# Optimization experiments

Measured on AMD Instinct MI355X. Metric: run time of the kernel, lower is better.

## Reference

```python
import jax, jax.numpy as jnp
import numpy as np

COMMITMENT_COST = 0.25


def setup_inputs() -> dict:
    key = jax.random.key(0)
    k1, k2 = jax.random.split(key)
    x = jax.random.normal(k1, (4, 64, 32, 32, 32), dtype=jnp.float32)
    weight = jax.random.normal(k2, (512, 64), dtype=jnp.float32)
    return {"x": x, "weight": weight}


def reference(x, weight):
    b, c, h, w, d = x.shape  # c == embed_dim
    # [b, h, w, d, c] -> [N, c]
    flat = jnp.transpose(x, (0, 2, 3, 4, 1)).reshape(-1, c)
    # squared L2 distances to each codebook vector: [N, n_embed]
    distances = (
        jnp.sum(flat * flat, axis=1, keepdims=True)
        - 2.0 * (flat @ weight.T)
        + jnp.sum(weight * weight, axis=1)
    )
    embed_idx_flat = jnp.argmin(distances, axis=1)  # == argmax(-distances)
    embed_idx = embed_idx_flat.reshape(b, h, w, d)
    # gather codebook rows and move embed dim back to channel position
    quantized = jnp.transpose(weight[embed_idx], (0, 4, 1, 2, 3))  # [b, c, h, w, d]
    latent_loss = COMMITMENT_COST * jnp.mean(
        (jax.lax.stop_gradient(quantized) - x) ** 2
    )
    quantized_st = jax.lax.stop_gradient(quantized - x) + x
    return quantized_st, embed_idx, latent_loss
```

## Files before the change

### kernel.cpp

```cpp
#include <hip/hip_runtime.h>
#include <hip/hip_bf16.h>

#define HWD      32768
#define NC       64
#define NE       512
#define OUT_IDX  8388608
#define OUT_LOSS 8519680

#define WS_WSQ_F   16
#define WS_SLOT_F  528
#define WS_WP_B    4096
#define WS_NEEDED  200704

typedef __attribute__((ext_vector_type(8))) short bf16x8;
typedef __attribute__((ext_vector_type(4))) float f32x4;

__device__ inline unsigned short bf16_rne(float v) {
    unsigned u = __builtin_bit_cast(unsigned, v);
    return (unsigned short)((u + 0x7FFFu + ((u >> 16) & 1u)) >> 16);
}
__device__ inline float bf16_f(unsigned short s) {
    return __builtin_bit_cast(float, (unsigned)s << 16);
}
__device__ inline void split3(float v, unsigned short& h, unsigned short& m,
                              unsigned short& l) {
    h = bf16_rne(v);
    float r1 = v - bf16_f(h);
    m = bf16_rne(r1);
    float r2 = r1 - bf16_f(m);
    l = bf16_rne(r2);
}

__global__ __launch_bounds__(256) void vq_prep(
    const float* __restrict__ w, float* __restrict__ ws)
{
    const int gtid = blockIdx.x * 256 + threadIdx.x;
    if (gtid == 0) { ws[0] = 0.f; ((unsigned*)ws)[1] = 0u; }
    if (gtid < 256) ws[WS_SLOT_F + gtid] = 0.f;
    if (gtid < NE) {
        const float4* row = (const float4*)(w + (size_t)gtid * NC);
        float s0 = 0.f, s1 = 0.f, s2 = 0.f, s3 = 0.f;
#pragma unroll
        for (int k = 0; k < 16; ++k) {
            float4 v = row[k];
            s0 = fmaf(v.x, v.x, s0); s1 = fmaf(v.y, v.y, s1);
            s2 = fmaf(v.z, v.z, s2); s3 = fmaf(v.w, v.w, s3);
        }
        ws[WS_WSQ_F + gtid] = (s0 + s1) + (s2 + s3);
    }
    const int lane_s = gtid & 63;
    int t = gtid >> 6;
    const int plane = t % 3; t /= 3;
    const int kc = t & 1;
    const int ct = t >> 1;
    const int code = ct * 16 + (lane_s & 15);
    const int kb   = kc * 32 + (lane_s >> 4) * 8;
    const float* src = w + (size_t)code * NC + kb;
    unsigned short o[8];
#pragma unroll
    for (int j = 0; j < 8; ++j) {
        unsigned short h, m, l;
        split3(src[j], h, m, l);
        o[j] = (plane == 0) ? h : (plane == 1) ? m : l;
    }
    unsigned short* dst = (unsigned short*)((char*)ws + WS_WP_B) + (size_t)gtid * 8;
#pragma unroll
    for (int j = 0; j < 8; ++j) dst[j] = o[j];
}

__device__ __forceinline__ void loadB(const bf16x8* __restrict__ wp,
                                      const float* __restrict__ wsqp,
                                      const int ct, const int lane,
                                      const int lanelo,
                                      bf16x8 (&B)[2][3], float& wsq)
{
#pragma unroll
    for (int kc = 0; kc < 2; ++kc)
#pragma unroll
        for (int p = 0; p < 3; ++p)
            B[kc][p] = wp[(size_t)((ct * 2 + kc) * 3 + p) * 64 + lane];
    wsq = wsqp[ct * 16 + lanelo];
}

__device__ __forceinline__ void tileUpd4(const bf16x8 (&A)[4][2][3],
                                         const bf16x8 (&B)[2][3],
                                         const float wsq, const int ct,
                                         const int lanelo,
                                         float (&best)[4][4], int (&bidx)[4][4])
{
    constexpr int AP[6] = {2, 1, 0, 1, 0, 0};
    constexpr int BP[6] = {0, 1, 2, 0, 1, 0};
    f32x4 acc[4];
#pragma unroll
    for (int pt = 0; pt < 4; ++pt) acc[pt] = (f32x4){0.f, 0.f, 0.f, 0.f};
#pragma unroll
    for (int s = 0; s < 12; ++s) {
        const int kc = s & 1, ap = AP[s >> 1], bp = BP[s >> 1];
#pragma unroll
        for (int pt = 0; pt < 4; ++pt)
            acc[pt] = __builtin_amdgcn_mfma_f32_16x16x32_bf16(
                A[pt][kc][ap], B[kc][bp], acc[pt], 0, 0, 0);
    }
#pragma unroll
    for (int pt = 0; pt < 4; ++pt)
#pragma unroll
        for (int r = 0; r < 4; ++r) {
            const float d = fmaf(-2.f, acc[pt][r], wsq);
            if (d < best[pt][r]) { best[pt][r] = d; bidx[pt][r] = ct * 16 + lanelo; }
        }
}

__global__ __launch_bounds__(256, 2) void vq_argmin(
    const float* __restrict__ x, float* __restrict__ ws,
    float* __restrict__ out)
{
    __shared__ int idx_sh[256];

    const int tid    = threadIdx.x;
    const int wv     = tid >> 6;
    const int lane   = tid & 63;
    const int lanelo = lane & 15;
    const int quad   = lane >> 4;
    const int posB   = blockIdx.x * 256;
    const int b      = posB >> 15;
    const int hwdB   = posB & (HWD - 1);
    const size_t xoff = (size_t)b * NC * HWD + hwdB;
    const int wpos   = wv * 64;

    const bf16x8* wp   = (const bf16x8*)((const char*)ws + WS_WP_B);
    const float*  wsqp = ws + WS_WSQ_F;

    bf16x8 B0[2][3], B1[2][3];
    float  w0, w1;
    loadB(wp, wsqp, 0, lane, lanelo, B0, w0);

    bf16x8 A[4][2][3];
#pragma unroll
    for (int pt = 0; pt < 4; ++pt) {
#pragma unroll
        for (int kc = 0; kc < 2; ++kc) {
            bf16x8 fh, fm, fl;
#pragma unroll
            for (int j = 0; j < 8; ++j) {
                const int k = kc * 32 + quad * 8 + j;
                const float v = x[xoff + (size_t)k * HWD + wpos + pt * 16 + lanelo];
                unsigned short h, m, l;
                split3(v, h, m, l);
                fh[j] = (short)h; fm[j] = (short)m; fl[j] = (short)l;
            }
            A[pt][kc][0] = fh; A[pt][kc][1] = fm; A[pt][kc][2] = fl;
        }
    }

    float best[4][4];
    int   bidx[4][4];
#pragma unroll
    for (int pt = 0; pt < 4; ++pt)
#pragma unroll
        for (int r = 0; r < 4; ++r) { best[pt][r] = 3.402823466e38f; bidx[pt][r] = 0; }

#pragma unroll 1
    for (int r = 0; r < 16; ++r) {
        const int ce = r * 2;
        loadB(wp, wsqp, ce + 1, lane, lanelo, B1, w1);
        tileUpd4(A, B0, w0, ce, lanelo, best, bidx);
        loadB(wp, wsqp, (ce + 2) & 31, lane, lanelo, B0, w0);
        tileUpd4(A, B1, w1, ce + 1, lanelo, best, bidx);
    }

#pragma unroll
    for (int pt = 0; pt < 4; ++pt)
#pragma unroll
        for (int r = 0; r < 4; ++r) {
            float d = best[pt][r]; int i = bidx[pt][r];
#pragma unroll
            for (int mlane = 1; mlane <= 8; mlane <<= 1) {
                const float d2 = __shfl_xor(d, mlane);
                const int   i2 = __shfl_xor(i, mlane);
                if (d2 < d || (d2 == d && i2 < i)) { d = d2; i = i2; }
            }
            if (lanelo == 0)
                idx_sh[wpos + pt * 16 + quad * 4 + r] = i;
        }
    __syncthreads();

    out[OUT_IDX + posB + tid] = (float)idx_sh[tid];
}

__global__ __launch_bounds__(256, 8) void vq_epilogue(
    const float* __restrict__ x, const float* __restrict__ w,
    float* __restrict__ ws, float* __restrict__ out)
{
    __shared__ float q_t[64 * 68];
    __shared__ int   idx_sh[64];
    __shared__ float wred[4];

    const int tid  = threadIdx.x;
    const int posB = blockIdx.x * 64;
    const int b    = posB >> 15;
    const int hwdB = posB & (HWD - 1);
    const size_t xoff = (size_t)b * NC * HWD + hwdB;

    if (tid < 64) idx_sh[tid] = (int)out[OUT_IDX + posB + tid];
    __syncthreads();

#pragma unroll
    for (int it = 0; it < 16; ++it) {
        const int e = it * 256 + tid;
        const int r = e >> 6, c = e & 63;
        q_t[c * 68 + r] = w[(size_t)idx_sh[r] * NC + c];
    }
    __syncthreads();

    float lsum = 0.f;
#pragma unroll
    for (int it = 0; it < 4; ++it) {
        const int s  = it * 256 + tid;
        const int c  = s >> 4;
        const int p0 = (s & 15) * 4;
        const size_t off = xoff + (size_t)c * HWD + p0;
        const float4 xv = *(const float4*)(x + off);
        const float4 qv = *(const float4*)(q_t + c * 68 + p0);
        const float dx = qv.x - xv.x, dy = qv.y - xv.y;
        const float dz = qv.z - xv.z, dw = qv.w - xv.w;
        lsum = fmaf(dx, dx, lsum); lsum = fmaf(dy, dy, lsum);
        lsum = fmaf(dz, dz, lsum); lsum = fmaf(dw, dw, lsum);
        float4 ov;
        ov.x = dx + xv.x; ov.y = dy + xv.y;
        ov.z = dz + xv.z; ov.w = dw + xv.w;
        *(float4*)(out + off) = ov;
    }

#pragma unroll
    for (int off = 32; off >= 1; off >>= 1) lsum += __shfl_down(lsum, off);
    if ((tid & 63) == 0) wred[tid >> 6] = lsum;
    __syncthreads();
    if (tid == 0)
        atomicAdd(ws + WS_SLOT_F + (blockIdx.x & 255),
                  (wred[0] + wred[1]) + (wred[2] + wred[3]));
}

__global__ __launch_bounds__(64) void vq_loss_fin(
    const float* __restrict__ ws, float* __restrict__ out)
{
    const int lane = threadIdx.x;
    float s = (ws[WS_SLOT_F + lane]       + ws[WS_SLOT_F + lane + 64]) +
              (ws[WS_SLOT_F + lane + 128] + ws[WS_SLOT_F + lane + 192]);
#pragma unroll
    for (int off = 32; off >= 1; off >>= 1) s += __shfl_down(s, off);
    if (lane == 0) out[OUT_LOSS] = 0.25f * s / 8388608.0f;
}

__global__ __launch_bounds__(256, 2) void vq_fused_fb(
    const float* __restrict__ x, const float* __restrict__ w,
    float* __restrict__ out, float* __restrict__ loss_acc)
{
    __shared__ float lw[256 * NC];
    __shared__ float wsq[256];
    __shared__ float wred[4];
    const int tid = threadIdx.x;
    const int n0  = blockIdx.x * 512;
    const int b   = n0 >> 15;
    const int hwd = (n0 & (HWD - 1)) + tid;
    const float* xp = x + (size_t)b * NC * HWD + hwd;
    float xr0[NC], xr1[NC];
#pragma unroll
    for (int c = 0; c < NC; ++c) { xr0[c] = xp[(size_t)c * HWD]; xr1[c] = xp[(size_t)c * HWD + 256]; }
    float xsq0 = 0.f, xsq1 = 0.f;
#pragma unroll
    for (int c = 0; c < NC; ++c) { xsq0 = fmaf(xr0[c], xr0[c], xsq0); xsq1 = fmaf(xr1[c], xr1[c], xsq1); }
    float best0 = 3.402823466e38f, best1 = 3.402823466e38f;
    int bi0 = 0, bi1 = 0;
    for (int pass = 0; pass < 2; ++pass) {
        if (pass) __syncthreads();
        const float4* wt = (const float4*)(w + pass * 256 * NC);
        float4* l4 = (float4*)lw;
#pragma unroll
        for (int k = 0; k < 16; ++k) l4[tid + k * 256] = wt[tid + k * 256];
        {
            const float4* row = wt + tid * 16;
            float s0 = 0.f, s1 = 0.f, s2 = 0.f, s3 = 0.f;
#pragma unroll
            for (int k = 0; k < 16; ++k) {
                float4 v = row[k];
                s0 = fmaf(v.x, v.x, s0); s1 = fmaf(v.y, v.y, s1);
                s2 = fmaf(v.z, v.z, s2); s3 = fmaf(v.w, v.w, s3);
            }
            wsq[tid] = (s0 + s1) + (s2 + s3);
        }
        __syncthreads();
#pragma unroll 2
        for (int e = 0; e < 256; ++e) {
            const float4* row = (const float4*)(lw + e * NC);
            float a0 = 0.f, a1 = 0.f, c0 = 0.f, c1 = 0.f;
#pragma unroll
            for (int k = 0; k < 16; ++k) {
                float4 v = row[k];
                a0 = fmaf(xr0[4 * k + 0], v.x, a0); a1 = fmaf(xr0[4 * k + 1], v.y, a1);
                a0 = fmaf(xr0[4 * k + 2], v.z, a0); a1 = fmaf(xr0[4 * k + 3], v.w, a1);
                c0 = fmaf(xr1[4 * k + 0], v.x, c0); c1 = fmaf(xr1[4 * k + 1], v.y, c1);
                c0 = fmaf(xr1[4 * k + 2], v.z, c0); c1 = fmaf(xr1[4 * k + 3], v.w, c1);
            }
            const float d0 = (xsq0 - 2.f * (a0 + a1)) + wsq[e];
            const float d1 = (xsq1 - 2.f * (c0 + c1)) + wsq[e];
            const int ge = pass * 256 + e;
            if (d0 < best0) { best0 = d0; bi0 = ge; }
            if (d1 < best1) { best1 = d1; bi1 = ge; }
        }
    }
    float* o0 = out + (size_t)b * NC * HWD + hwd;
    float lsum = 0.f;
    const float4* r0 = (const float4*)(w + bi0 * NC);
    const float4* r1 = (const float4*)(w + bi1 * NC);
#pragma unroll
    for (int k = 0; k < 16; ++k) {
        float4 q0 = r0[k], q1 = r1[k];
        float qv0[4] = { q0.x, q0.y, q0.z, q0.w };
        float qv1[4] = { q1.x, q1.y, q1.z, q1.w };
#pragma unroll
        for (int j = 0; j < 4; ++j) {
            const int c = 4 * k + j;
            const float dv0 = qv0[j] - xr0[c];
            const float dv1 = qv1[j] - xr1[c];
            lsum = fmaf(dv0, dv0, lsum); lsum = fmaf(dv1, dv1, lsum);
            o0[(size_t)c * HWD] = dv0 + xr0[c];
            o0[(size_t)c * HWD + 256] = dv1 + xr1[c];
        }
    }
    const int n = b * HWD + hwd;
    out[OUT_IDX + n] = (float)bi0;
    out[OUT_IDX + n + 256] = (float)bi1;
#pragma unroll
    for (int off = 32; off >= 1; off >>= 1) lsum += __shfl_down(lsum, off);
    if ((tid & 63) == 0) wred[tid >> 6] = lsum;
    __syncthreads();
    if (tid == 0) atomicAdd(loss_acc, (wred[0] + wred[1]) + (wred[2] + wred[3]));
}

__global__ void vq_loss_fin_fb(const float* __restrict__ acc, float* __restrict__ out)
{
    out[OUT_LOSS] = 0.25f * acc[0] / 8388608.0f;
}

extern "C" void kernel_launch(void* const* d_in, const int* in_sizes, int n_in,
                              void* d_out, int out_size, void* d_ws, size_t ws_size,
                              hipStream_t stream)
{
    const float* x = (const float*)d_in[0];
    const float* w = (const float*)d_in[1];
    float* out = (float*)d_out;
    float* ws  = (float*)d_ws;

    if (ws_size >= WS_NEEDED) {
        vq_prep<<<48, 256, 0, stream>>>(w, ws);
        vq_argmin<<<512, 256, 0, stream>>>(x, ws, out);
        vq_epilogue<<<2048, 256, 0, stream>>>(x, w, ws, out);
        vq_loss_fin<<<1, 64, 0, stream>>>(ws, out);
    } else {
        hipMemsetAsync(d_ws, 0, sizeof(float), stream);
        vq_fused_fb<<<256, 256, 0, stream>>>(x, w, out, ws);
        vq_loss_fin_fb<<<1, 1, 0, stream>>>(ws, out);
    }
}
```

Before: 135.3 us.

## Switch argmin distance GEMM to 32x32x16 MFMA with 32-position waves

Rewrites the distance computation to use 32x32x16 bf16 MFMA tiles instead of four 16x16x32 tiles, repacking the codebook split planes in the prep kernel to match. Each wave now handles 32 positions against 32-code tiles, with two alternating accumulators to hide MFMA dependency latency. The grid doubles to 1024 blocks of 128 positions. This aims to cut MFMA issue count and B-operand reloads per FLOP, at the cost of fewer positions per block, more blocks re-reading the codebook, and a wider shuffle reduction.

Measured after the change: 154.0 us. 1.14x slower.

```diff
diff --git a/kernel.cpp b/kernel.cpp
--- a/kernel.cpp
+++ b/kernel.cpp
@@ -12,8 +12,9 @@
 #define WS_WP_B    4096
 #define WS_NEEDED  200704
 
-typedef __attribute__((ext_vector_type(8))) short bf16x8;
-typedef __attribute__((ext_vector_type(4))) float f32x4;
+typedef __attribute__((ext_vector_type(8)))  short bf16x8;
+typedef __attribute__((ext_vector_type(4)))  float f32x4;
+typedef __attribute__((ext_vector_type(16))) float f32x16;
 
 __device__ inline unsigned short bf16_rne(float v) {
     unsigned u = __builtin_bit_cast(unsigned, v);
@@ -49,12 +50,12 @@
         ws[WS_WSQ_F + gtid] = (s0 + s1) + (s2 + s3);
     }
     const int lane_s = gtid & 63;
-    int t = gtid >> 6;
-    const int plane = t % 3; t /= 3;
-    const int kc = t & 1;
-    const int ct = t >> 1;
-    const int code = ct * 16 + (lane_s & 15);
-    const int kb   = kc * 32 + (lane_s >> 4) * 8;
+    int f = gtid >> 6;
+    const int plane = f % 3; f /= 3;
+    const int kc4 = f & 3;
+    const int ct  = f >> 2;
+    const int code = ct * 32 + (lane_s & 31);
+    const int kb   = kc4 * 16 + (lane_s >> 5) * 8;
     const float* src = w + (size_t)code * NC + kb;
     unsigned short o[8];
 #pragma unroll
@@ -68,123 +69,122 @@
     for (int j = 0; j < 8; ++j) dst[j] = o[j];
 }
 
-__device__ __forceinline__ void loadB(const bf16x8* __restrict__ wp,
-                                      const float* __restrict__ wsqp,
-                                      const int ct, const int lane,
-                                      const int lanelo,
-                                      bf16x8 (&B)[2][3], float& wsq)
-{
-#pragma unroll
-    for (int kc = 0; kc < 2; ++kc)
+__device__ __forceinline__ void loadB32(const bf16x8* __restrict__ wp,
+                                        const float* __restrict__ wsqp,
+                                        const int ct, const int lane,
+                                        const int lane31,
+                                        bf16x8 (&B)[4][3], float& wsq)
+{
+#pragma unroll
+    for (int kc4 = 0; kc4 < 4; ++kc4)
 #pragma unroll
         for (int p = 0; p < 3; ++p)
-            B[kc][p] = wp[(size_t)((ct * 2 + kc) * 3 + p) * 64 + lane];
-    wsq = wsqp[ct * 16 + lanelo];
-}
-
-__device__ __forceinline__ void tileUpd4(const bf16x8 (&A)[4][2][3],
-                                         const bf16x8 (&B)[2][3],
-                                         const float wsq, const int ct,
-                                         const int lanelo,
-                                         float (&best)[4][4], int (&bidx)[4][4])
+            B[kc4][p] = wp[(size_t)((ct * 4 + kc4) * 3 + p) * 64 + lane];
+    wsq = wsqp[ct * 32 + lane31];
+}
+
+__device__ __forceinline__ void mfmaTile(const bf16x8 (&A)[4][3],
+                                         const bf16x8 (&B)[4][3],
+                                         f32x16& acc)
 {
     constexpr int AP[6] = {2, 1, 0, 1, 0, 0};
     constexpr int BP[6] = {0, 1, 2, 0, 1, 0};
-    f32x4 acc[4];
-#pragma unroll
-    for (int pt = 0; pt < 4; ++pt) acc[pt] = (f32x4){0.f, 0.f, 0.f, 0.f};
-#pragma unroll
-    for (int s = 0; s < 12; ++s) {
-        const int kc = s & 1, ap = AP[s >> 1], bp = BP[s >> 1];
-#pragma unroll
-        for (int pt = 0; pt < 4; ++pt)
-            acc[pt] = __builtin_amdgcn_mfma_f32_16x16x32_bf16(
-                A[pt][kc][ap], B[kc][bp], acc[pt], 0, 0, 0);
-    }
-#pragma unroll
-    for (int pt = 0; pt < 4; ++pt)
-#pragma unroll
-        for (int r = 0; r < 4; ++r) {
-            const float d = fmaf(-2.f, acc[pt][r], wsq);
-            if (d < best[pt][r]) { best[pt][r] = d; bidx[pt][r] = ct * 16 + lanelo; }
-        }
+    f32x16 a0 = {0.f,0.f,0.f,0.f,0.f,0.f,0.f,0.f,0.f,0.f,0.f,0.f,0.f,0.f,0.f,0.f};
+    f32x16 a1 = {0.f,0.f,0.f,0.f,0.f,0.f,0.f,0.f,0.f,0.f,0.f,0.f,0.f,0.f,0.f,0.f};
+#pragma unroll
+    for (int c = 0; c < 6; ++c) {
+        a0 = __builtin_amdgcn_mfma_f32_32x32x16_bf16(A[0][AP[c]], B[0][BP[c]], a0, 0, 0, 0);
+        a1 = __builtin_amdgcn_mfma_f32_32x32x16_bf16(A[1][AP[c]], B[1][BP[c]], a1, 0, 0, 0);
+        a0 = __builtin_amdgcn_mfma_f32_32x32x16_bf16(A[2][AP[c]], B[2][BP[c]], a0, 0, 0, 0);
+        a1 = __builtin_amdgcn_mfma_f32_32x32x16_bf16(A[3][AP[c]], B[3][BP[c]], a1, 0, 0, 0);
+    }
+    acc = a0 + a1;
+}
+
+__device__ __forceinline__ void bestUpd(const f32x16& acc, const float wsq,
+                                        const int ct, const int lane31,
+                                        float (&best)[16], int (&bidx)[16])
+{
+#pragma unroll
+    for (int r = 0; r < 16; ++r) {
+        const float d = fmaf(-2.f, acc[r], wsq);
+        if (d < best[r]) { best[r] = d; bidx[r] = ct * 32 + lane31; }
+    }
 }
 
 __global__ __launch_bounds__(256, 2) void vq_argmin(
     const float* __restrict__ x, float* __restrict__ ws,
     float* __restrict__ out)
 {
-    __shared__ int idx_sh[256];
+    __shared__ int idx_sh[128];
 
     const int tid    = threadIdx.x;
     const int wv     = tid >> 6;
     const int lane   = tid & 63;
-    const int lanelo = lane & 15;
-    const int quad   = lane >> 4;
-    const int posB   = blockIdx.x * 256;
+    const int lane31 = lane & 31;
+    const int hi     = lane >> 5;
+    const int posB   = blockIdx.x * 128;
     const int b      = posB >> 15;
     const int hwdB   = posB & (HWD - 1);
     const size_t xoff = (size_t)b * NC * HWD + hwdB;
-    const int wpos   = wv * 64;
+    const int wpos   = wv * 32;
 
     const bf16x8* wp   = (const bf16x8*)((const char*)ws + WS_WP_B);
     const float*  wsqp = ws + WS_WSQ_F;
 
-    bf16x8 B0[2][3], B1[2][3];
+    bf16x8 B0[4][3], B1[4][3];
     float  w0, w1;
-    loadB(wp, wsqp, 0, lane, lanelo, B0, w0);
-
-    bf16x8 A[4][2][3];
-#pragma unroll
-    for (int pt = 0; pt < 4; ++pt) {
-#pragma unroll
-        for (int kc = 0; kc < 2; ++kc) {
-            bf16x8 fh, fm, fl;
-#pragma unroll
-            for (int j = 0; j < 8; ++j) {
-                const int k = kc * 32 + quad * 8 + j;
-                const float v = x[xoff + (size_t)k * HWD + wpos + pt * 16 + lanelo];
-                unsigned short h, m, l;
-                split3(v, h, m, l);
-                fh[j] = (short)h; fm[j] = (short)m; fl[j] = (short)l;
-            }
-            A[pt][kc][0] = fh; A[pt][kc][1] = fm; A[pt][kc][2] = fl;
-        }
-    }
-
-    float best[4][4];
-    int   bidx[4][4];
-#pragma unroll
-    for (int pt = 0; pt < 4; ++pt)
-#pragma unroll
-        for (int r = 0; r < 4; ++r) { best[pt][r] = 3.402823466e38f; bidx[pt][r] = 0; }
+    loadB32(wp, wsqp, 0, lane, lane31, B0, w0);
+    loadB32(wp, wsqp, 1, lane, lane31, B1, w1);
+
+    bf16x8 A[4][3];
+#pragma unroll
+    for (int kc4 = 0; kc4 < 4; ++kc4) {
+        bf16x8 fh, fm, fl;
+#pragma unroll
+        for (int j = 0; j < 8; ++j) {
+            const int k = kc4 * 16 + hi * 8 + j;
+            const float v = x[xoff + (size_t)k * HWD + wpos + lane31];
+            unsigned short h, m, l;
+            split3(v, h, m, l);
+            fh[j] = (short)h; fm[j] = (short)m; fl[j] = (short)l;
+        }
+        A[kc4][0] = fh; A[kc4][1] = fm; A[kc4][2] = fl;
+    }
+
+    float best[16];
+    int   bidx[16];
+#pragma unroll
+    for (int r = 0; r < 16; ++r) { best[r] = 3.402823466e38f; bidx[r] = 0; }
 
 #pragma unroll 1
+    for (int r8 = 0; r8 < 8; ++r8) {
+        const int te = r8 * 2;
+        f32x16 accE, accO;
+        const float wsqE = w0, wsqO = w1;
+        mfmaTile(A, B0, accE);
+        loadB32(wp, wsqp, (te + 2) & 15, lane, lane31, B0, w0);
+        bestUpd(accE, wsqE, te, lane31, best, bidx);
+        mfmaTile(A, B1, accO);
+        loadB32(wp, wsqp, (te + 3) & 15, lane, lane31, B1, w1);
+        bestUpd(accO, wsqO, te + 1, lane31, best, bidx);
+    }
+
+#pragma unroll
     for (int r = 0; r < 16; ++r) {
-        const int ce = r * 2;
-        loadB(wp, wsqp, ce + 1, lane, lanelo, B1, w1);
-        tileUpd4(A, B0, w0, ce, lanelo, best, bidx);
-        loadB(wp, wsqp, (ce + 2) & 31, lane, lanelo, B0, w0);
-        tileUpd4(A, B1, w1, ce + 1, lanelo, best, bidx);
-    }
-
-#pragma unroll
-    for (int pt = 0; pt < 4; ++pt)
-#pragma unroll
-        for (int r = 0; r < 4; ++r) {
-            float d = best[pt][r]; int i = bidx[pt][r];
-#pragma unroll
-            for (int mlane = 1; mlane <= 8; mlane <<= 1) {
-                const float d2 = __shfl_xor(d, mlane);
-                const int   i2 = __shfl_xor(i, mlane);
-                if (d2 < d || (d2 == d && i2 < i)) { d = d2; i = i2; }
-            }
-            if (lanelo == 0)
-                idx_sh[wpos + pt * 16 + quad * 4 + r] = i;
-        }
-    __syncthreads();
-
-    out[OUT_IDX + posB + tid] = (float)idx_sh[tid];
+        float d = best[r]; int i = bidx[r];
+#pragma unroll
+        for (int mlane = 1; mlane <= 16; mlane <<= 1) {
+            const float d2 = __shfl_xor(d, mlane);
+            const int   i2 = __shfl_xor(i, mlane);
+            if (d2 < d || (d2 == d && i2 < i)) { d = d2; i = i2; }
+        }
+        if (lane31 == 0)
+            idx_sh[wpos + (r & 3) + 8 * (r >> 2) + 4 * hi] = i;
+    }
+    __syncthreads();
+
+    if (tid < 128) out[OUT_IDX + posB + tid] = (float)idx_sh[tid];
 }
 
 __global__ __launch_bounds__(256, 8) void vq_epilogue(
@@ -353,7 +353,7 @@
 
     if (ws_size >= WS_NEEDED) {
         vq_prep<<<48, 256, 0, stream>>>(w, ws);
-        vq_argmin<<<512, 256, 0, stream>>>(x, ws, out);
+        vq_argmin<<<1024, 256, 0, stream>>>(x, ws, out);
         vq_epilogue<<<2048, 256, 0, stream>>>(x, w, ws, out);
         vq_loss_fin<<<1, 64, 0, stream>>>(ws, out);
     } else {
```
